# Optimization experiments

Hardware: AMD Instinct MI355X
Metric: run time of the kernel (lower is better)

The kernel has to match this reference:

```python
import jax, jax.numpy as jnp
import numpy as np

IN_CH = 32
OUT_CH = 32
M1, M2 = 32, 32
BS, H, W = 8, 256, 256


def setup_inputs() -> dict:
    key = jax.random.key(0)
    kx, kk = jax.random.split(key)
    x = jax.random.normal(kx, (BS, IN_CH, H, W), dtype=jnp.float32)
    # reset_parameters: randn * (1/(in_ch*out_ch)) + 1
    scale = 1.0 / (IN_CH * OUT_CH)
    kernel = jax.random.normal(kk, (2, 1, OUT_CH, M1, M2, 2), dtype=jnp.float32) * scale + 1.0
    r = jnp.float32(1.0)
    return {"x": x, "kernel": kernel, "r": r}


def reference(x, kernel, r):
    # view_as_complex: last dim of 2 -> complex, shape [2, 1, C, M1, M2]
    kc = (kernel[..., 0] + 1j * kernel[..., 1]).astype(jnp.complex64)
    # elementwise complex power kernel**r
    kc = jnp.power(kc, r)

    # forward 2D real FFT over spatial dims (ortho norm)
    x_ft = jnp.fft.rfftn(x, axes=(-2, -1), norm="ortho")  # [bs, C, H, W//2+1]
    Hf, Wr = x_ft.shape[-2], x_ft.shape[-1]
    n1 = min(Hf // 2, M1)
    n2 = min(Wr, M2)

    def mix(block, k):
        # fft over channel dim (-3), multiply by complex kernel, ifft back
        b = jnp.fft.fft(block, axis=-3, norm="ortho")
        b = b * k[..., :n1, :n2]
        return jnp.fft.ifft(b, axis=-3, norm="ortho")

    pos = mix(x_ft[..., :n1, :n2], kc[0])          # low positive freqs
    neg = mix(x_ft[..., Hf - n1:, :n2], kc[1])     # low negative freqs

    out_ft = jnp.zeros((x.shape[0], OUT_CH, Hf, Wr), dtype=jnp.complex64)
    out_ft = out_ft.at[..., :n1, :n2].set(pos)
    out_ft = out_ft.at[..., Hf - n1:, :n2].set(neg)

    # inverse real FFT back to spatial domain
    return jnp.fft.irfftn(out_ft, s=(x.shape[-2], x.shape[-1]), axes=(-2, -1), norm="ortho")
```

## Files before the change

### kernel.cpp

```cpp
#include <hip/hip_runtime.h>
#include <math.h>


#define TWO_PI 6.28318530717958647692f

__global__ __launch_bounds__(256) void kP(const float* __restrict__ kin,
                                          const float* __restrict__ rp,
                                          float2* __restrict__ kp) {
  const int i = blockIdx.x * 256 + threadIdx.x;
  const float r = rp[0];
  const float kr = kin[2 * i], ki = kin[2 * i + 1];
  const float m2 = fmaf(kr, kr, ki * ki);
  float2 o = make_float2(0.f, 0.f);
  if (m2 > 0.f) {
    const float lm = 0.5f * logf(m2);
    const float ang = atan2f(ki, kr);
    const float mag = expf(r * lm);
    float s, c;
    sincosf(r * ang, &s, &c);
    o = make_float2(mag * c, mag * s);
  }
  kp[i] = o;
}

__global__ __launch_bounds__(256) void kA(const float* __restrict__ x,
                                          float2* __restrict__ z1) {
  __shared__ float xs[8192];
  const int tid = threadIdx.x;
  const long row0 = (long)blockIdx.x * 32;
  const float* xg = x + row0 * 256;
  {
    const int xl = tid & 31, rq = tid >> 5;
    const float* xgr = xg + rq * 4 * 256 + xl;
#pragma unroll
    for (int cb = 0; cb < 8; ++cb) {
      const int xc = xl + 32 * cb;
      const float4 v = make_float4(xgr[32 * cb], xgr[32 * cb + 256],
                                   xgr[32 * cb + 512], xgr[32 * cb + 768]);
      *(float4*)(xs + xc * 32 + 4 * ((rq + xc) & 7)) = v;
    }
  }
  __syncthreads();
  for (int i = tid; i < 127 * 32; i += 256) {
    const int xi = 1 + (i >> 5), r = i & 31;
    const int ai = (xi << 5) + ((r + 4 * xi) & 31);
    const int bi = ((256 - xi) << 5) + ((r - 4 * xi) & 31);
    const float a = xs[ai], b = xs[bi];
    xs[ai] = a + b;
    xs[bi] = a - b;
  }
  __syncthreads();
  const int w = tid & 31;
  const int r0 = (tid >> 5) << 2;
  int uo[8];
#pragma unroll
  for (int j = 0; j < 8; ++j) uo[j] = ((r0 + 4 * j) & 31) << 2;
  const float sgn = (w & 1) ? -1.f : 1.f;
  const float4 x0 = *(const float4*)(xs + r0);
  const float4 x128 = *(const float4*)(xs + (128 << 5) + r0);
  float Cr0 = fmaf(sgn, x128.x, x0.x), Cr1 = fmaf(sgn, x128.y, x0.y);
  float Cr2 = fmaf(sgn, x128.z, x0.z), Cr3 = fmaf(sgn, x128.w, x0.w);
  float Ci0 = 0, Ci1 = 0, Ci2 = 0, Ci3 = 0;
  float s1, c1;
  sincosf(TWO_PI * (float)w / 256.0f, &s1, &c1);
  float pc = c1, ps = s1;
  const char* const xsb = (const char*)xs;
#define KA_BODY(UPTR, VPTR)                                        \
  {                                                                \
    const float4 u = *(const float4*)(UPTR);                       \
    const float4 v = *(const float4*)(VPTR);                       \
    Cr0 = fmaf(u.x, pc, Cr0); Ci0 = fmaf(-v.x, ps, Ci0);           \
    Cr1 = fmaf(u.y, pc, Cr1); Ci1 = fmaf(-v.y, ps, Ci1);           \
    Cr2 = fmaf(u.z, pc, Cr2); Ci2 = fmaf(-v.z, ps, Ci2);           \
    Cr3 = fmaf(u.w, pc, Cr3); Ci3 = fmaf(-v.w, ps, Ci3);           \
    const float tn = fmaf(pc, c1, -ps * s1);                       \
    ps = fmaf(pc, s1, ps * c1);                                    \
    pc = tn;                                                       \
  }
  {
    const char* ub = xsb;
    const char* vb = xsb + 249 * 128;
#pragma unroll
    for (int j = 1; j < 8; ++j)
      KA_BODY(ub + j * 128 + uo[j], vb + (7 - j) * 128 + uo[8 - j])
  }
  for (int xb = 8; xb <= 120; xb += 8) {
    const char* ub = xsb + xb * 128;
    const char* vb = xsb + (249 - xb) * 128;
#pragma unroll
    for (int j = 0; j < 8; ++j)
      KA_BODY(ub + j * 128 + uo[j], vb + (7 - j) * 128 + uo[(8 - j) & 7])
  }
#undef KA_BODY
  float2* o = z1 + (row0 + r0) * 32 + w;
  o[0]  = make_float2(Cr0, Ci0);
  o[32] = make_float2(Cr1, Ci1);
  o[64] = make_float2(Cr2, Ci2);
  o[96] = make_float2(Cr3, Ci3);
}

__global__ __launch_bounds__(256) void kB(const float2* __restrict__ z1,
                                          float2* __restrict__ z2p) {
  __shared__ float2 zs[128 * 32];
  const int bc = blockIdx.x >> 1, yh = blockIdx.x & 1;
  const float2* src = z1 + (long)bc * 8192 + yh * 4096;
  for (int i = threadIdx.x; i < 4096; i += 256) zs[i] = src[i];
  __syncthreads();
  const int t = threadIdx.x >> 2, wq = threadIdx.x & 3;
  const int h = (t < 32) ? t : (192 + t);
  float sr, cr;
  sincosf(-TWO_PI * (float)h / 256.0f, &sr, &cr);
  float pc = (yh && (t & 1)) ? -1.f : 1.f, ps = 0.f;
  float ar[8], ai[8];
#pragma unroll
  for (int k = 0; k < 8; ++k) { ar[k] = 0.f; ai[k] = 0.f; }
  const float* zb = (const float*)zs + wq * 16;
#pragma unroll 2
  for (int y = 0; y < 128; ++y) {
    const float4* zf = (const float4*)(zb + y * 64);
#pragma unroll
    for (int k = 0; k < 4; ++k) {
      const float4 q = zf[k];
      ar[2 * k]     = fmaf(q.x, pc, fmaf(-q.y, ps, ar[2 * k]));
      ai[2 * k]     = fmaf(q.x, ps, fmaf( q.y, pc, ai[2 * k]));
      ar[2 * k + 1] = fmaf(q.z, pc, fmaf(-q.w, ps, ar[2 * k + 1]));
      ai[2 * k + 1] = fmaf(q.z, ps, fmaf( q.w, pc, ai[2 * k + 1]));
    }
    const float tn = fmaf(pc, cr, -ps * sr);
    ps = fmaf(pc, sr, ps * cr);
    pc = tn;
  }
  float4* dst = (float4*)(z2p + (long)yh * 524288 + (long)bc * 2048 + t * 32 + wq * 8);
#pragma unroll
  for (int k = 0; k < 4; ++k)
    dst[k] = make_float4(ar[2 * k], ai[2 * k], ar[2 * k + 1], ai[2 * k + 1]);
}

__global__ __launch_bounds__(256) void kC(const float2* __restrict__ z2a,
                                          const float2* __restrict__ z2b,
                                          const float2* __restrict__ kp,
                                          float2* __restrict__ g) {
  __shared__ float2 z2s[16 * 33];
  __shared__ float2 fk[16 * 33];
  __shared__ float2 tw[32];
  const int tid = threadIdx.x;
  if (tid < 32) {
    float s, c;
    sincosf(-TWO_PI * (float)tid / 32.0f, &s, &c);
    tw[tid] = make_float2(c, s);
  }
  const int m0 = blockIdx.x * 16;
  const int b = m0 >> 11;
  const int twi = m0 & 2047;
  const int t = twi >> 5;
  const int w0 = twi & 31;
  const int s_ = t >> 5, tm = t & 31;
  for (int i = tid; i < 512; i += 256) {
    const int ci = i >> 4, wj = i & 15;
    const long idx = ((long)(b * 32 + ci)) * 2048 + t * 32 + w0 + wj;
    const float2 va = z2a[idx], vb = z2b[idx];
    z2s[wj * 33 + ci] = make_float2(va.x + vb.x, va.y + vb.y);
  }
  __syncthreads();
  const int m = tid & 15;
  const int p = tid >> 4;
  const int cf0 = 2 * p, cf1 = 2 * p + 1;
  {
    float f0r = 0, f0i = 0, f1r = 0, f1i = 0;
    int i0 = 0, i1 = 0;
#pragma unroll 8
    for (int ci = 0; ci < 32; ++ci) {
      const float2 z = z2s[m * 33 + ci];
      const float2 t0 = tw[i0]; i0 = (i0 + cf0) & 31;
      const float2 t1 = tw[i1]; i1 = (i1 + cf1) & 31;
      f0r = fmaf(z.x, t0.x, fmaf(-z.y, t0.y, f0r));
      f0i = fmaf(z.x, t0.y, fmaf( z.y, t0.x, f0i));
      f1r = fmaf(z.x, t1.x, fmaf(-z.y, t1.y, f1r));
      f1i = fmaf(z.x, t1.y, fmaf( z.y, t1.x, f1i));
    }
    const float2 k0 = kp[((s_ * 32 + cf0) * 32 + tm) * 32 + w0 + m];
    const float2 k1 = kp[((s_ * 32 + cf1) * 32 + tm) * 32 + w0 + m];
    fk[m * 33 + cf0] = make_float2(f0r * k0.x - f0i * k0.y, f0r * k0.y + f0i * k0.x);
    fk[m * 33 + cf1] = make_float2(f1r * k1.x - f1i * k1.y, f1r * k1.y + f1i * k1.x);
  }
  __syncthreads();
  {
    float g0r = 0, g0i = 0, g1r = 0, g1i = 0;
    int i0 = 0, i1 = 0;
    const int co0 = 2 * p, co1 = 2 * p + 1;
#pragma unroll 8
    for (int cf = 0; cf < 32; ++cf) {
      const float2 f = fk[m * 33 + cf];
      const float2 t0 = tw[i0]; i0 = (i0 + co0) & 31;
      const float2 t1 = tw[i1]; i1 = (i1 + co1) & 31;
      g0r = fmaf(f.x, t0.x, fmaf( f.y, t0.y, g0r));
      g0i = fmaf(f.y, t0.x, fmaf(-f.x, t0.y, g0i));
      g1r = fmaf(f.x, t1.x, fmaf( f.y, t1.y, g1r));
      g1i = fmaf(f.y, t1.x, fmaf(-f.x, t1.y, g1i));
    }
    const float SC = 1.0f / 8192.0f;
    g[((long)(b * 32 + co0)) * 2048 + t * 32 + w0 + m] = make_float2(g0r * SC, g0i * SC);
    g[((long)(b * 32 + co1)) * 2048 + t * 32 + w0 + m] = make_float2(g1r * SC, g1i * SC);
  }
}

__global__ __launch_bounds__(256) void kDE(const float2* __restrict__ g,
                                           float* __restrict__ out) {
  __shared__ float2 gs[2048];
  __shared__ float2 tst[32 * 34];
  const int tid = threadIdx.x;
  const int bc = blockIdx.x >> 3, yq = blockIdx.x & 7;
  const float2* src = g + (long)bc * 2048;
  for (int i = tid; i < 2048; i += 256) gs[i] = src[i];
  __syncthreads();
  {
    const int y5 = tid >> 3, wq = tid & 7;
    const int y = yq * 32 + y5;
    float s1, c1;
    sincosf(TWO_PI * (float)y / 256.0f, &s1, &c1);
    float Tr[4], Ti[4];
#pragma unroll
    for (int k = 0; k < 4; ++k) { Tr[k] = 0.f; Ti[k] = 0.f; }
    float pc = 1.f, ps = 0.f;
    const float* gb = (const float*)gs + wq * 8;
    for (int t = 0; t < 64; ++t) {
      if (t == 32) {
        float s2, c2;
        sincosf(TWO_PI * (float)((224 * y) & 255) / 256.0f, &s2, &c2);
        pc = c2; ps = s2;
      }
      const float4* gf = (const float4*)(gb + t * 64);
      const float4 qa = gf[0], qb = gf[1];
      Tr[0] = fmaf(qa.x, pc, fmaf(-qa.y, ps, Tr[0]));
      Ti[0] = fmaf(qa.x, ps, fmaf( qa.y, pc, Ti[0]));
      Tr[1] = fmaf(qa.z, pc, fmaf(-qa.w, ps, Tr[1]));
      Ti[1] = fmaf(qa.z, ps, fmaf( qa.w, pc, Ti[1]));
      Tr[2] = fmaf(qb.x, pc, fmaf(-qb.y, ps, Tr[2]));
      Ti[2] = fmaf(qb.x, ps, fmaf( qb.y, pc, Ti[2]));
      Tr[3] = fmaf(qb.z, pc, fmaf(-qb.w, ps, Tr[3]));
      Ti[3] = fmaf(qb.z, ps, fmaf( qb.w, pc, Ti[3]));
      const float tn = fmaf(pc, c1, -ps * s1);
      ps = fmaf(pc, s1, ps * c1);
      pc = tn;
    }
#pragma unroll
    for (int k = 0; k < 4; ++k) {
      const int w = wq * 4 + k;
      const float sc = w ? (2.0f / 256.0f) : (1.0f / 256.0f);
      tst[w * 34 + y5] = make_float2(Tr[k] * sc, Ti[k] * sc);
    }
  }
  __syncthreads();
  {
    const int xq = tid & 31;
    const int rh = tid >> 5;
    float sb, cb;
    sincosf(TWO_PI * (float)xq / 256.0f, &sb, &cb);
    const float RT = 0.70710678118654752440f;
    const float stc1 = RT * (cb - sb), sts1 = RT * (cb + sb);
    const float stc[4] = {cb, stc1, -sb, -sts1};
    const float sts[4] = {sb, sts1, cb, stc1};
    float C[4][4], S[4][4];
#pragma unroll
    for (int m = 0; m < 4; ++m)
#pragma unroll
      for (int j = 0; j < 4; ++j) { C[m][j] = 0.f; S[m][j] = 0.f; }
    float pc[4] = {1.f, 1.f, 1.f, 1.f}, ps[4] = {0.f, 0.f, 0.f, 0.f};
    const float* tbse = (const float*)tst + rh * 8;
#pragma unroll 2
    for (int w = 0; w < 32; ++w) {
      const float4 q0 = *(const float4*)(tbse + w * 68);
      const float4 q1 = *(const float4*)(tbse + w * 68 + 4);
#pragma unroll
      for (int m = 0; m < 4; ++m) {
        C[m][0] = fmaf(q0.x, pc[m], C[m][0]);
        S[m][0] = fmaf(q0.y, ps[m], S[m][0]);
        C[m][1] = fmaf(q0.z, pc[m], C[m][1]);
        S[m][1] = fmaf(q0.w, ps[m], S[m][1]);
        C[m][2] = fmaf(q1.x, pc[m], C[m][2]);
        S[m][2] = fmaf(q1.y, ps[m], S[m][2]);
        C[m][3] = fmaf(q1.z, pc[m], C[m][3]);
        S[m][3] = fmaf(q1.w, ps[m], S[m][3]);
        const float tn = fmaf(pc[m], stc[m], -ps[m] * sts[m]);
        ps[m] = fmaf(pc[m], sts[m], ps[m] * stc[m]);
        pc[m] = tn;
      }
    }
    const long rbase = (long)bc * 256 + yq * 32;
#pragma unroll
    for (int m = 0; m < 4; ++m) {
      const int xx = xq + 32 * m;
#pragma unroll
      for (int j = 0; j < 4; ++j) {
        const long row = rbase + rh * 4 + j;
        out[row * 256 + xx] = C[m][j] - S[m][j];
        out[row * 256 + ((256 - xx) & 255)] = C[m][j] + S[m][j];
      }
    }
    if (tid < 32) {
      float ae = 0.f, ao = 0.f;
#pragma unroll
      for (int k = 0; k < 16; ++k) {
        ae += tst[(2 * k) * 34 + tid].x;
        ao += tst[(2 * k + 1) * 34 + tid].x;
      }
      out[(rbase + tid) * 256 + 128] = ae - ao;
    }
  }
}

extern "C" void kernel_launch(void* const* d_in, const int* in_sizes, int n_in,
                              void* d_out, int out_size, void* d_ws, size_t ws_size,
                              hipStream_t stream) {
  const float* x = (const float*)d_in[0];
  const float* kin = (const float*)d_in[1];
  const float* rp = (const float*)d_in[2];
  float* out = (float*)d_out;
  char* ws = (char*)d_ws;

  float2* z1  = (float2*)(ws);
  float2* z2a = (float2*)(ws + (16ull << 20));
  float2* kp  = (float2*)(ws + (24ull << 20));
  float2* g   = (float2*)(ws);

  kP<<<256, 256, 0, stream>>>(kin, rp, kp);
  kA<<<2048, 256, 0, stream>>>(x, z1);
  kB<<<512, 256, 0, stream>>>(z1, z2a);
  kC<<<1024, 256, 0, stream>>>(z2a, z2a + 524288, kp, g);
  kDE<<<2048, 256, 0, stream>>>(g, out);
}
```

Measured before the change: 210.3 us.

## Factor row-direction DFTs into radix-8 and radix-32 stages across new kernels

Splits the 256-point column DFT in kB into an in-place radix-8 butterfly pass (kB1) followed by a 32-point twiddled DFT (kB2). Likewise splits the inverse DFT over the 64 retained frequency rows into kD1 (partial sums per y1) plus an 8-point combine in kDE. This cuts the arithmetic per output from a direct 256-term or 64-term sum to a factored form. In exchange it adds two kernel launches and extra global-memory round trips through z1 and a new U buffer.

```diff
diff --git a/kernel.cpp b/kernel.cpp
--- a/kernel.cpp
+++ b/kernel.cpp
@@ -99,45 +99,67 @@
   o[96] = make_float2(Cr3, Ci3);
 }
 
-__global__ __launch_bounds__(256) void kB(const float2* __restrict__ z1,
-                                          float2* __restrict__ z2p) {
-  __shared__ float2 zs[128 * 32];
-  const int bc = blockIdx.x >> 1, yh = blockIdx.x & 1;
-  const float2* src = z1 + (long)bc * 8192 + yh * 4096;
-  for (int i = threadIdx.x; i < 4096; i += 256) zs[i] = src[i];
-  __syncthreads();
-  const int t = threadIdx.x >> 2, wq = threadIdx.x & 3;
+__global__ __launch_bounds__(256) void kB1(float2* __restrict__ z1) {
+  const int gt = blockIdx.x * 256 + threadIdx.x;
+  const int w = gt & 31, y1 = (gt >> 5) & 31, bc = gt >> 10;
+  float2* base = z1 + (long)bc * 8192 + y1 * 32 + w;
+  float2 a[8];
+#pragma unroll
+  for (int j = 0; j < 8; ++j) a[j] = base[j * 1024];
+  float2 t0 = make_float2(a[0].x + a[4].x, a[0].y + a[4].y);
+  float2 t1 = make_float2(a[0].x - a[4].x, a[0].y - a[4].y);
+  float2 t2 = make_float2(a[2].x + a[6].x, a[2].y + a[6].y);
+  float2 t3 = make_float2(a[2].x - a[6].x, a[2].y - a[6].y);
+  const float2 E0 = make_float2(t0.x + t2.x, t0.y + t2.y);
+  const float2 E2 = make_float2(t0.x - t2.x, t0.y - t2.y);
+  const float2 E1 = make_float2(t1.x + t3.y, t1.y - t3.x);
+  const float2 E3 = make_float2(t1.x - t3.y, t1.y + t3.x);
+  t0 = make_float2(a[1].x + a[5].x, a[1].y + a[5].y);
+  t1 = make_float2(a[1].x - a[5].x, a[1].y - a[5].y);
+  t2 = make_float2(a[3].x + a[7].x, a[3].y + a[7].y);
+  t3 = make_float2(a[3].x - a[7].x, a[3].y - a[7].y);
+  const float2 O0 = make_float2(t0.x + t2.x, t0.y + t2.y);
+  const float2 O2 = make_float2(t0.x - t2.x, t0.y - t2.y);
+  const float2 O1 = make_float2(t1.x + t3.y, t1.y - t3.x);
+  const float2 O3 = make_float2(t1.x - t3.y, t1.y + t3.x);
+  const float RT = 0.70710678118654752440f;
+  const float2 B0 = O0;
+  const float2 B1 = make_float2(RT * (O1.x + O1.y), RT * (O1.y - O1.x));
+  const float2 B2 = make_float2(O2.y, -O2.x);
+  const float2 B3 = make_float2(RT * (O3.y - O3.x), -RT * (O3.x + O3.y));
+  base[0]        = make_float2(E0.x + B0.x, E0.y + B0.y);
+  base[1 * 1024] = make_float2(E1.x + B1.x, E1.y + B1.y);
+  base[2 * 1024] = make_float2(E2.x + B2.x, E2.y + B2.y);
+  base[3 * 1024] = make_float2(E3.x + B3.x, E3.y + B3.y);
+  base[4 * 1024] = make_float2(E0.x - B0.x, E0.y - B0.y);
+  base[5 * 1024] = make_float2(E1.x - B1.x, E1.y - B1.y);
+  base[6 * 1024] = make_float2(E2.x - B2.x, E2.y - B2.y);
+  base[7 * 1024] = make_float2(E3.x - B3.x, E3.y - B3.y);
+}
+
+__global__ __launch_bounds__(256) void kB2(const float2* __restrict__ s,
+                                           float2* __restrict__ z2) {
+  const int bc = blockIdx.x >> 3, tq = blockIdx.x & 7;
+  const int k = threadIdx.x >> 5, w = threadIdx.x & 31;
+  const int t = tq * 8 + k;
   const int h = (t < 32) ? t : (192 + t);
   float sr, cr;
   sincosf(-TWO_PI * (float)h / 256.0f, &sr, &cr);
-  float pc = (yh && (t & 1)) ? -1.f : 1.f, ps = 0.f;
-  float ar[8], ai[8];
-#pragma unroll
-  for (int k = 0; k < 8; ++k) { ar[k] = 0.f; ai[k] = 0.f; }
-  const float* zb = (const float*)zs + wq * 16;
-#pragma unroll 2
-  for (int y = 0; y < 128; ++y) {
-    const float4* zf = (const float4*)(zb + y * 64);
-#pragma unroll
-    for (int k = 0; k < 4; ++k) {
-      const float4 q = zf[k];
-      ar[2 * k]     = fmaf(q.x, pc, fmaf(-q.y, ps, ar[2 * k]));
-      ai[2 * k]     = fmaf(q.x, ps, fmaf( q.y, pc, ai[2 * k]));
-      ar[2 * k + 1] = fmaf(q.z, pc, fmaf(-q.w, ps, ar[2 * k + 1]));
-      ai[2 * k + 1] = fmaf(q.z, ps, fmaf( q.w, pc, ai[2 * k + 1]));
-    }
+  const float2* src = s + (long)bc * 8192 + k * 1024 + w;
+  float ar = 0.f, ai = 0.f;
+  float pc = 1.f, ps = 0.f;
+  for (int y1 = 0; y1 < 32; ++y1) {
+    const float2 v = src[y1 * 32];
+    ar = fmaf(v.x, pc, fmaf(-v.y, ps, ar));
+    ai = fmaf(v.x, ps, fmaf( v.y, pc, ai));
     const float tn = fmaf(pc, cr, -ps * sr);
     ps = fmaf(pc, sr, ps * cr);
     pc = tn;
   }
-  float4* dst = (float4*)(z2p + (long)yh * 524288 + (long)bc * 2048 + t * 32 + wq * 8);
-#pragma unroll
-  for (int k = 0; k < 4; ++k)
-    dst[k] = make_float4(ar[2 * k], ai[2 * k], ar[2 * k + 1], ai[2 * k + 1]);
-}
-
-__global__ __launch_bounds__(256) void kC(const float2* __restrict__ z2a,
-                                          const float2* __restrict__ z2b,
+  z2[(long)bc * 2048 + t * 32 + w] = make_float2(ar, ai);
+}
+
+__global__ __launch_bounds__(256) void kC(const float2* __restrict__ z2,
                                           const float2* __restrict__ kp,
                                           float2* __restrict__ g) {
   __shared__ float2 z2s[16 * 33];
@@ -158,8 +180,7 @@
   for (int i = tid; i < 512; i += 256) {
     const int ci = i >> 4, wj = i & 15;
     const long idx = ((long)(b * 32 + ci)) * 2048 + t * 32 + w0 + wj;
-    const float2 va = z2a[idx], vb = z2b[idx];
-    z2s[wj * 33 + ci] = make_float2(va.x + vb.x, va.y + vb.y);
+    z2s[wj * 33 + ci] = z2[idx];
   }
   __syncthreads();
   const int m = tid & 15;
@@ -204,50 +225,71 @@
   }
 }
 
-__global__ __launch_bounds__(256) void kDE(const float2* __restrict__ g,
+__global__ __launch_bounds__(256) void kD1(const float2* __restrict__ g,
+                                           float2* __restrict__ U) {
+  const int bc = blockIdx.x >> 3, y1q = blockIdx.x & 7;
+  const int p = threadIdx.x >> 5, w = threadIdx.x & 31;
+  const float2* gb = g + (long)bc * 2048 + w;
+  float2* ub = U + (long)bc * 8192 + p * 32 + w;
+#pragma unroll
+  for (int y1l = 0; y1l < 4; ++y1l) {
+    const int y1 = y1q * 4 + y1l;
+    float st, ct;
+    sincosf(TWO_PI * (float)y1 / 32.0f, &st, &ct);
+    float s1, c1;
+    sincosf(TWO_PI * (float)((p * y1) & 255) / 256.0f, &s1, &c1);
+    float s2, c2;
+    sincosf(TWO_PI * (float)(((224 + p) * y1) & 255) / 256.0f, &s2, &c2);
+    float ar = 0.f, ai = 0.f;
+    float pc = c1, ps = s1, qc = c2, qs = s2;
+#pragma unroll
+    for (int j = 0; j < 4; ++j) {
+      const float2 va = gb[(p + 8 * j) * 32];
+      const float2 vb = gb[(32 + p + 8 * j) * 32];
+      ar = fmaf(va.x, pc, fmaf(-va.y, ps, ar));
+      ai = fmaf(va.x, ps, fmaf( va.y, pc, ai));
+      ar = fmaf(vb.x, qc, fmaf(-vb.y, qs, ar));
+      ai = fmaf(vb.x, qs, fmaf( vb.y, qc, ai));
+      const float tn = fmaf(pc, ct, -ps * st);
+      ps = fmaf(pc, st, ps * ct);
+      pc = tn;
+      const float tm = fmaf(qc, ct, -qs * st);
+      qs = fmaf(qc, st, qs * ct);
+      qc = tm;
+    }
+    ub[y1 * 256] = make_float2(ar, ai);
+  }
+}
+
+__global__ __launch_bounds__(256) void kDE(const float2* __restrict__ U,
                                            float* __restrict__ out) {
-  __shared__ float2 gs[2048];
   __shared__ float2 tst[32 * 34];
   const int tid = threadIdx.x;
   const int bc = blockIdx.x >> 3, yq = blockIdx.x & 7;
-  const float2* src = g + (long)bc * 2048;
-  for (int i = tid; i < 2048; i += 256) gs[i] = src[i];
-  __syncthreads();
   {
     const int y5 = tid >> 3, wq = tid & 7;
-    const int y = yq * 32 + y5;
-    float s1, c1;
-    sincosf(TWO_PI * (float)y / 256.0f, &s1, &c1);
-    float Tr[4], Ti[4];
-#pragma unroll
-    for (int k = 0; k < 4; ++k) { Tr[k] = 0.f; Ti[k] = 0.f; }
-    float pc = 1.f, ps = 0.f;
-    const float* gb = (const float*)gs + wq * 8;
-    for (int t = 0; t < 64; ++t) {
-      if (t == 32) {
-        float s2, c2;
-        sincosf(TWO_PI * (float)((224 * y) & 255) / 256.0f, &s2, &c2);
-        pc = c2; ps = s2;
-      }
-      const float4* gf = (const float4*)(gb + t * 64);
-      const float4 qa = gf[0], qb = gf[1];
-      Tr[0] = fmaf(qa.x, pc, fmaf(-qa.y, ps, Tr[0]));
-      Ti[0] = fmaf(qa.x, ps, fmaf( qa.y, pc, Ti[0]));
-      Tr[1] = fmaf(qa.z, pc, fmaf(-qa.w, ps, Tr[1]));
-      Ti[1] = fmaf(qa.z, ps, fmaf( qa.w, pc, Ti[1]));
-      Tr[2] = fmaf(qb.x, pc, fmaf(-qb.y, ps, Tr[2]));
-      Ti[2] = fmaf(qb.x, ps, fmaf( qb.y, pc, Ti[2]));
-      Tr[3] = fmaf(qb.z, pc, fmaf(-qb.w, ps, Tr[3]));
-      Ti[3] = fmaf(qb.z, ps, fmaf( qb.w, pc, Ti[3]));
-      const float tn = fmaf(pc, c1, -ps * s1);
-      ps = fmaf(pc, s1, ps * c1);
-      pc = tn;
-    }
-#pragma unroll
-    for (int k = 0; k < 4; ++k) {
-      const int w = wq * 4 + k;
+    const float* ub = (const float*)(U + (long)bc * 8192 + (long)y5 * 256 + wq * 4);
+    float Tr[4] = {0.f, 0.f, 0.f, 0.f}, Ti[4] = {0.f, 0.f, 0.f, 0.f};
+#pragma unroll
+    for (int p = 0; p < 8; ++p) {
+      float sp, cp;
+      sincosf(TWO_PI * (float)((p * yq) & 7) / 8.0f, &sp, &cp);
+      const float4 qa = *(const float4*)(ub + p * 64);
+      const float4 qb = *(const float4*)(ub + p * 64 + 4);
+      Tr[0] = fmaf(qa.x, cp, fmaf(-qa.y, sp, Tr[0]));
+      Ti[0] = fmaf(qa.x, sp, fmaf( qa.y, cp, Ti[0]));
+      Tr[1] = fmaf(qa.z, cp, fmaf(-qa.w, sp, Tr[1]));
+      Ti[1] = fmaf(qa.z, sp, fmaf( qa.w, cp, Ti[1]));
+      Tr[2] = fmaf(qb.x, cp, fmaf(-qb.y, sp, Tr[2]));
+      Ti[2] = fmaf(qb.x, sp, fmaf( qb.y, cp, Ti[2]));
+      Tr[3] = fmaf(qb.z, cp, fmaf(-qb.w, sp, Tr[3]));
+      Ti[3] = fmaf(qb.z, sp, fmaf( qb.w, cp, Ti[3]));
+    }
+#pragma unroll
+    for (int kk = 0; kk < 4; ++kk) {
+      const int w = wq * 4 + kk;
       const float sc = w ? (2.0f / 256.0f) : (1.0f / 256.0f);
-      tst[w * 34 + y5] = make_float2(Tr[k] * sc, Ti[k] * sc);
+      tst[w * 34 + y5] = make_float2(Tr[kk] * sc, Ti[kk] * sc);
     }
   }
   __syncthreads();
@@ -318,14 +360,17 @@
   float* out = (float*)d_out;
   char* ws = (char*)d_ws;
 
-  float2* z1  = (float2*)(ws);
-  float2* z2a = (float2*)(ws + (16ull << 20));
-  float2* kp  = (float2*)(ws + (24ull << 20));
-  float2* g   = (float2*)(ws);
+  float2* z1 = (float2*)(ws);
+  float2* z2 = (float2*)(ws + (16ull << 20));
+  float2* kp = (float2*)(ws + (24ull << 20));
+  float2* g  = (float2*)(ws);
+  float2* U  = (float2*)(ws + (4ull << 20));
 
   kP<<<256, 256, 0, stream>>>(kin, rp, kp);
   kA<<<2048, 256, 0, stream>>>(x, z1);
-  kB<<<512, 256, 0, stream>>>(z1, z2a);
-  kC<<<1024, 256, 0, stream>>>(z2a, z2a + 524288, kp, g);
-  kDE<<<2048, 256, 0, stream>>>(g, out);
-}
+  kB1<<<1024, 256, 0, stream>>>(z1);
+  kB2<<<2048, 256, 0, stream>>>(z1, z2);
+  kC<<<1024, 256, 0, stream>>>(z2, kp, g);
+  kD1<<<2048, 256, 0, stream>>>(g, U);
+  kDE<<<2048, 256, 0, stream>>>(U, out);
+}
```

New measurement: 217.0 us. +3.2%, slower.
